# Optimization experiments

Measured on AMD Instinct MI355X. Metric: run time of the kernel, lower is better.

## Reference

```python
import jax, jax.numpy as jnp
import numpy as np

N_FEATURES = 128
D_EMBED = 64
GRID_SIZE = 5
SPLINE_ORDER = 3
FOURIER_GRIDSIZE = 10
GRID_RANGE = (-1.0, 1.0)


def setup_inputs() -> dict:
    key = jax.random.key(0)
    k1, k2, k3, k4 = jax.random.split(key, 4)
    b = 8192
    x = jax.random.uniform(k1, (b, N_FEATURES), dtype=jnp.float32)
    # grid buffer: (n_features, grid_size + 2*spline_order + 1)
    h = (GRID_RANGE[1] - GRID_RANGE[0]) / GRID_SIZE
    grid_1d = jnp.arange(-SPLINE_ORDER, GRID_SIZE + SPLINE_ORDER + 1, dtype=jnp.float32) * h + GRID_RANGE[0]
    grid = jnp.broadcast_to(grid_1d, (N_FEATURES, grid_1d.shape[0]))
    # parameters (random stand-ins for the torch init)
    base_weight = jax.random.normal(k2, (N_FEATURES, D_EMBED), dtype=jnp.float32) * 0.1
    spline_weight = jax.random.normal(k3, (N_FEATURES, D_EMBED, GRID_SIZE + SPLINE_ORDER), dtype=jnp.float32) * 0.02
    spline_scaler = jax.random.normal(k4, (N_FEATURES, D_EMBED), dtype=jnp.float32) * 0.1
    kf1, kf2 = jax.random.split(jax.random.fold_in(key, 7))
    fourier_coeffs = jax.random.normal(kf1, (2, N_FEATURES, D_EMBED, FOURIER_GRIDSIZE), dtype=jnp.float32) / (
        np.sqrt(N_FEATURES) * np.sqrt(FOURIER_GRIDSIZE))
    fourier_bias = jnp.zeros((1, N_FEATURES, D_EMBED), dtype=jnp.float32)
    return {
        'x': x, 'grid': grid, 'base_weight': base_weight,
        'spline_weight': spline_weight, 'spline_scaler': spline_scaler,
        'fourier_coeffs': fourier_coeffs, 'fourier_bias': fourier_bias,
    }


def b_splines(x, grid):
    # x: (b, n), grid: (n, grid_size + 2*spline_order + 1)
    xb = x[..., None]  # (b, n, 1)
    bases = ((xb >= grid[:, :-1]) & (xb < grid[:, 1:])).astype(x.dtype)  # (b, n, G+2k)
    for k in range(1, SPLINE_ORDER + 1):  # Cox-de Boor recursion (fixed small order)
        left = (xb - grid[:, :-(k + 1)]) / (grid[:, k:-1] - grid[:, :-(k + 1)])
        right = (grid[:, k + 1:] - xb) / (grid[:, k + 1:] - grid[:, 1:-k])
        bases = left * bases[:, :, :-1] + right * bases[:, :, 1:]
    return bases  # (b, n, grid_size + spline_order)


def reference(x, grid, base_weight, spline_weight, spline_scaler, fourier_coeffs, fourier_bias):
    # base branch: SiLU(x) outer-broadcast with per-feature weight -> (b, n, d)
    base_out = jax.nn.silu(x)[..., None] * base_weight[None]
    # spline branch
    bases = b_splines(x, grid)  # (b, n, i) with i = grid_size + spline_order
    scaled_w = spline_weight * spline_scaler[..., None]  # (n, d, i)
    spline_out = jnp.einsum('bni,ndi->bnd', bases, scaled_w)
    # Fourier branch: sum_g cos(k_g x) c0[n,d,g] + sin(k_g x) c1[n,d,g]
    kvec = jnp.arange(1, FOURIER_GRIDSIZE + 1, dtype=x.dtype)
    ang = x[..., None] * kvec  # (b, n, g)
    fourier_out = (jnp.einsum('bng,ndg->bnd', jnp.cos(ang), fourier_coeffs[0])
                   + jnp.einsum('bng,ndg->bnd', jnp.sin(ang), fourier_coeffs[1])
                   + fourier_bias)
    return base_out + spline_out + fourier_out
```

## Files before the change

kernel.cpp:

```cpp
#include <hip/hip_runtime.h>
#include <math.h>

#define NF   128
#define DE   64
#define GS   5
#define SO   3
#define FG   10
#define NG   12
#define NB0  11
#define NBF  8
#define WREC 32

__global__ __launch_bounds__(256)
void kan_prep(const float* __restrict__ grid,
              const float* __restrict__ bw, const float* __restrict__ sw,
              const float* __restrict__ ss, const float* __restrict__ fc,
              const float* __restrict__ fb,
              float* __restrict__ W, float* __restrict__ INV) {
  int idx = blockIdx.x * blockDim.x + threadIdx.x;
  if (idx >= NF * DE) return;
  int n = idx >> 6, d = idx & 63;
  (void)d;
  float* w = W + (size_t)idx * WREC;
  w[0] = bw[idx];
  w[1] = fb[idx];
  float s = ss[idx];
  const float* swp = sw + (size_t)idx * NBF;
#pragma unroll
  for (int i = 0; i < NBF; ++i) w[2 + i] = swp[i] * s;
  const float* f0 = fc + (size_t)idx * FG;
  const float* f1 = fc + (size_t)(NF * DE + idx) * FG;
#pragma unroll
  for (int g = 0; g < FG; ++g) { w[10 + g] = f0[g]; w[20 + g] = f1[g]; }
  w[30] = 0.f; w[31] = 0.f;
  if (d == 0) {
    const float* g_ = grid + n * NG;
    float* iv = INV + n * 32;
    int o = 0;
#pragma unroll
    for (int k = 1; k <= SO; ++k)
      for (int j = 0; j + k < NG; ++j)
        iv[o++] = 1.0f / (g_[j + k] - g_[j]);
    iv[30] = 0.f; iv[31] = 0.f;
  }
}

template <bool PACKED>
__global__ __launch_bounds__(256)
void kan_main(const float* __restrict__ x, const float* __restrict__ grid,
              const float* __restrict__ bw, const float* __restrict__ sw,
              const float* __restrict__ ss, const float* __restrict__ fc,
              const float* __restrict__ fb,
              const float* __restrict__ W, const float* __restrict__ INV,
              float* __restrict__ out, int B) {
  const int n = blockIdx.x;
  const int wv = threadIdx.x >> 6;
  const int lane = threadIdx.x & 63;
  const int b = ((blockIdx.y * 4 + wv) << 6) + lane;
  if (b >= B) return;

  const float xv = x[(size_t)b * NF + n];

  float g[NG];
#pragma unroll
  for (int j = 0; j < NG; ++j) g[j] = grid[n * NG + j];

  const float sil = xv / (1.0f + expf(-xv));

  float bs[NB0];
#pragma unroll
  for (int j = 0; j < NB0; ++j)
    bs[j] = (xv >= g[j] && xv < g[j + 1]) ? 1.0f : 0.0f;

  if (PACKED) {
    const float* iv = INV + n * 32;
    const float* iv1 = iv;
    const float* iv2 = iv + 11;
    const float* iv3 = iv + 21;
#pragma unroll
    for (int j = 0; j < 10; ++j) {
      float left  = (xv - g[j]) * iv1[j];
      float right = (g[j + 2] - xv) * iv1[j + 1];
      bs[j] = left * bs[j] + right * bs[j + 1];
    }
#pragma unroll
    for (int j = 0; j < 9; ++j) {
      float left  = (xv - g[j]) * iv2[j];
      float right = (g[j + 3] - xv) * iv2[j + 1];
      bs[j] = left * bs[j] + right * bs[j + 1];
    }
#pragma unroll
    for (int j = 0; j < 8; ++j) {
      float left  = (xv - g[j]) * iv3[j];
      float right = (g[j + 4] - xv) * iv3[j + 1];
      bs[j] = left * bs[j] + right * bs[j + 1];
    }
  } else {
#pragma unroll
    for (int k = 1; k <= SO; ++k) {
      for (int j = 0; j < NB0 - k; ++j) {
        float left  = (xv - g[j]) / (g[j + k] - g[j]);
        float right = (g[j + k + 1] - xv) / (g[j + k + 1] - g[j + 1]);
        bs[j] = left * bs[j] + right * bs[j + 1];
      }
    }
  }

  float cs[FG], sn[FG];
  float s1, c1;
  sincosf(xv, &s1, &c1);
  cs[0] = c1; sn[0] = s1;
#pragma unroll
  for (int gi = 1; gi < FG; ++gi) {
    float cp = cs[gi - 1], sp = sn[gi - 1];
    cs[gi] = cp * c1 - sp * s1;
    sn[gi] = sp * c1 + cp * s1;
  }

  float4* outp = reinterpret_cast<float4*>(out + ((size_t)b * NF + n) * DE);

  if (PACKED) {
    const float* wp = W + (size_t)n * DE * WREC;
    for (int d4 = 0; d4 < DE / 4; ++d4) {
      float4 o;
#pragma unroll
      for (int q = 0; q < 4; ++q) {
        const float* w = wp + (size_t)(d4 * 4 + q) * WREC;
        float a = fmaf(sil, w[0], w[1]);
#pragma unroll
        for (int i = 0; i < NBF; ++i) a = fmaf(bs[i], w[2 + i], a);
#pragma unroll
        for (int gi = 0; gi < FG; ++gi) a = fmaf(cs[gi], w[10 + gi], a);
#pragma unroll
        for (int gi = 0; gi < FG; ++gi) a = fmaf(sn[gi], w[20 + gi], a);
        (&o.x)[q] = a;
      }
      outp[d4] = o;
    }
  } else {
    const float* bwp = bw + n * DE;
    const float* fbp = fb + n * DE;
    const float* ssp = ss + n * DE;
    const float* swp = sw + (size_t)n * DE * NBF;
    const float* f0  = fc + (size_t)n * DE * FG;
    const float* f1  = fc + (size_t)(NF + n) * DE * FG;
    for (int d4 = 0; d4 < DE / 4; ++d4) {
      float4 o;
#pragma unroll
      for (int q = 0; q < 4; ++q) {
        int d = d4 * 4 + q;
        float a = fmaf(sil, bwp[d], fbp[d]);
        float scl = ssp[d];
#pragma unroll
        for (int i = 0; i < NBF; ++i) a = fmaf(bs[i] * scl, swp[d * NBF + i], a);
#pragma unroll
        for (int gi = 0; gi < FG; ++gi) a = fmaf(cs[gi], f0[d * FG + gi], a);
#pragma unroll
        for (int gi = 0; gi < FG; ++gi) a = fmaf(sn[gi], f1[d * FG + gi], a);
        (&o.x)[q] = a;
      }
      outp[d4] = o;
    }
  }
}

extern "C" void kernel_launch(void* const* d_in, const int* in_sizes, int n_in,
                              void* d_out, int out_size, void* d_ws, size_t ws_size,
                              hipStream_t stream) {
  const float* x    = (const float*)d_in[0];
  const float* grid = (const float*)d_in[1];
  const float* bw   = (const float*)d_in[2];
  const float* sw   = (const float*)d_in[3];
  const float* ss   = (const float*)d_in[4];
  const float* fc   = (const float*)d_in[5];
  const float* fb   = (const float*)d_in[6];
  float* out = (float*)d_out;

  const int B = in_sizes[0] / NF;
  dim3 mgrid(NF, (unsigned)((B + 255) / 256));
  const size_t need = (size_t)(NF * DE * WREC + NF * 32) * sizeof(float);

  if (ws_size >= need) {
    float* W   = (float*)d_ws;
    float* INV = W + (size_t)NF * DE * WREC;
    kan_prep<<<(NF * DE + 255) / 256, 256, 0, stream>>>(grid, bw, sw, ss, fc, fb, W, INV);
    kan_main<true><<<mgrid, 256, 0, stream>>>(x, grid, bw, sw, ss, fc, fb, W, INV, out, B);
  } else {
    kan_main<false><<<mgrid, 256, 0, stream>>>(x, grid, bw, sw, ss, fc, fb,
                                               nullptr, nullptr, out, B);
  }
}
```

Measured before the change: 429.5 us.

## Split KAN into feature-row kernel and coalesced per-dimension dot kernel

```diff
diff --git a/kernel.cpp b/kernel.cpp
--- a/kernel.cpp
+++ b/kernel.cpp
@@ -10,6 +10,8 @@
 #define NB0  11
 #define NBF  8
 #define WREC 32
+#define BPW  128
+
 
 __global__ __launch_bounds__(256)
 void kan_prep(const float* __restrict__ grid,
@@ -45,67 +47,139 @@
   }
 }
 
-template <bool PACKED>
 __global__ __launch_bounds__(256)
-void kan_main(const float* __restrict__ x, const float* __restrict__ grid,
+void kan_scal(const float* __restrict__ x, const float* __restrict__ grid,
+              const float* __restrict__ INV, float* __restrict__ S, int B) {
+  const int n = blockIdx.x;
+  const int b = blockIdx.y * 256 + threadIdx.x;
+  if (b >= B) return;
+
+  const float xv = x[(size_t)b * NF + n];
+
+  float g[NG];
+#pragma unroll
+  for (int j = 0; j < NG; ++j) g[j] = grid[n * NG + j];
+
+  const float sil = xv / (1.0f + expf(-xv));
+
+  float bs[NB0];
+#pragma unroll
+  for (int j = 0; j < NB0; ++j)
+    bs[j] = (xv >= g[j] && xv < g[j + 1]) ? 1.0f : 0.0f;
+
+  const float* iv = INV + n * 32;
+  const float* iv1 = iv;
+  const float* iv2 = iv + 11;
+  const float* iv3 = iv + 21;
+#pragma unroll
+  for (int j = 0; j < 10; ++j) {
+    float left  = (xv - g[j]) * iv1[j];
+    float right = (g[j + 2] - xv) * iv1[j + 1];
+    bs[j] = left * bs[j] + right * bs[j + 1];
+  }
+#pragma unroll
+  for (int j = 0; j < 9; ++j) {
+    float left  = (xv - g[j]) * iv2[j];
+    float right = (g[j + 3] - xv) * iv2[j + 1];
+    bs[j] = left * bs[j] + right * bs[j + 1];
+  }
+#pragma unroll
+  for (int j = 0; j < 8; ++j) {
+    float left  = (xv - g[j]) * iv3[j];
+    float right = (g[j + 4] - xv) * iv3[j + 1];
+    bs[j] = left * bs[j] + right * bs[j + 1];
+  }
+
+  float cs[FG], sn[FG];
+  float s1, c1;
+  sincosf(xv, &s1, &c1);
+  cs[0] = c1; sn[0] = s1;
+#pragma unroll
+  for (int gi = 1; gi < FG; ++gi) {
+    float cp = cs[gi - 1], sp = sn[gi - 1];
+    cs[gi] = cp * c1 - sp * s1;
+    sn[gi] = sp * c1 + cp * s1;
+  }
+
+  float r[WREC];
+  r[0] = sil; r[1] = 1.0f;
+#pragma unroll
+  for (int j = 0; j < NBF; ++j) r[2 + j] = bs[j];
+#pragma unroll
+  for (int gi = 0; gi < FG; ++gi) { r[10 + gi] = cs[gi]; r[20 + gi] = sn[gi]; }
+  r[30] = 0.f; r[31] = 0.f;
+
+  float4* sp4 = reinterpret_cast<float4*>(S + ((size_t)b * NF + n) * WREC);
+#pragma unroll
+  for (int q = 0; q < 8; ++q)
+    sp4[q] = make_float4(r[q * 4 + 0], r[q * 4 + 1], r[q * 4 + 2], r[q * 4 + 3]);
+}
+
+__global__ __launch_bounds__(256, 8)
+void kan_dot(const float* __restrict__ W, const float* __restrict__ S,
+             float* __restrict__ out, int B) {
+  const int n = blockIdx.x;
+  const int wv = __builtin_amdgcn_readfirstlane(threadIdx.x >> 6);
+  const int lane = threadIdx.x & 63;
+  const int bstart = (blockIdx.y * 4 + wv) * BPW;
+  if (bstart >= B) return;
+  const int nb = (B - bstart < BPW) ? (B - bstart) : BPW;
+
+  float wr[WREC];
+  const float4* wq = reinterpret_cast<const float4*>(W + ((size_t)n * DE + lane) * WREC);
+#pragma unroll
+  for (int q = 0; q < 8; ++q) {
+    float4 t = wq[q];
+    wr[q * 4 + 0] = t.x; wr[q * 4 + 1] = t.y; wr[q * 4 + 2] = t.z; wr[q * 4 + 3] = t.w;
+  }
+
+  const float* sp = S + ((size_t)bstart * NF + n) * WREC;
+  float* op = out + ((size_t)bstart * NF + n) * DE + lane;
+
+  for (int i = 0; i < nb; ++i) {
+    float a0 = 0.f, a1 = 0.f, a2 = 0.f, a3 = 0.f;
+#pragma unroll
+    for (int j = 0; j < 28; j += 4) {
+      a0 = fmaf(sp[j + 0], wr[j + 0], a0);
+      a1 = fmaf(sp[j + 1], wr[j + 1], a1);
+      a2 = fmaf(sp[j + 2], wr[j + 2], a2);
+      a3 = fmaf(sp[j + 3], wr[j + 3], a3);
+    }
+    a0 = fmaf(sp[28], wr[28], a0);
+    a1 = fmaf(sp[29], wr[29], a1);
+    *op = (a0 + a1) + (a2 + a3);
+    sp += (size_t)NF * WREC;
+    op += (size_t)NF * DE;
+  }
+}
+
+__global__ __launch_bounds__(256)
+void kan_mono(const float* __restrict__ x, const float* __restrict__ grid,
               const float* __restrict__ bw, const float* __restrict__ sw,
               const float* __restrict__ ss, const float* __restrict__ fc,
-              const float* __restrict__ fb,
-              const float* __restrict__ W, const float* __restrict__ INV,
-              float* __restrict__ out, int B) {
+              const float* __restrict__ fb, float* __restrict__ out, int B) {
   const int n = blockIdx.x;
   const int wv = threadIdx.x >> 6;
   const int lane = threadIdx.x & 63;
   const int b = ((blockIdx.y * 4 + wv) << 6) + lane;
   if (b >= B) return;
-
   const float xv = x[(size_t)b * NF + n];
-
   float g[NG];
 #pragma unroll
   for (int j = 0; j < NG; ++j) g[j] = grid[n * NG + j];
-
   const float sil = xv / (1.0f + expf(-xv));
-
   float bs[NB0];
 #pragma unroll
   for (int j = 0; j < NB0; ++j)
     bs[j] = (xv >= g[j] && xv < g[j + 1]) ? 1.0f : 0.0f;
-
-  if (PACKED) {
-    const float* iv = INV + n * 32;
-    const float* iv1 = iv;
-    const float* iv2 = iv + 11;
-    const float* iv3 = iv + 21;
-#pragma unroll
-    for (int j = 0; j < 10; ++j) {
-      float left  = (xv - g[j]) * iv1[j];
-      float right = (g[j + 2] - xv) * iv1[j + 1];
+#pragma unroll
+  for (int k = 1; k <= SO; ++k) {
+    for (int j = 0; j < NB0 - k; ++j) {
+      float left  = (xv - g[j]) / (g[j + k] - g[j]);
+      float right = (g[j + k + 1] - xv) / (g[j + k + 1] - g[j + 1]);
       bs[j] = left * bs[j] + right * bs[j + 1];
     }
-#pragma unroll
-    for (int j = 0; j < 9; ++j) {
-      float left  = (xv - g[j]) * iv2[j];
-      float right = (g[j + 3] - xv) * iv2[j + 1];
-      bs[j] = left * bs[j] + right * bs[j + 1];
-    }
-#pragma unroll
-    for (int j = 0; j < 8; ++j) {
-      float left  = (xv - g[j]) * iv3[j];
-      float right = (g[j + 4] - xv) * iv3[j + 1];
-      bs[j] = left * bs[j] + right * bs[j + 1];
-    }
-  } else {
-#pragma unroll
-    for (int k = 1; k <= SO; ++k) {
-      for (int j = 0; j < NB0 - k; ++j) {
-        float left  = (xv - g[j]) / (g[j + k] - g[j]);
-        float right = (g[j + k + 1] - xv) / (g[j + k + 1] - g[j + 1]);
-        bs[j] = left * bs[j] + right * bs[j + 1];
-      }
-    }
-  }
-
+  }
   float cs[FG], sn[FG];
   float s1, c1;
   sincosf(xv, &s1, &c1);
@@ -116,51 +190,29 @@
     cs[gi] = cp * c1 - sp * s1;
     sn[gi] = sp * c1 + cp * s1;
   }
-
+  const float* bwp = bw + n * DE;
+  const float* fbp = fb + n * DE;
+  const float* ssp = ss + n * DE;
+  const float* swp = sw + (size_t)n * DE * NBF;
+  const float* f0  = fc + (size_t)n * DE * FG;
+  const float* f1  = fc + (size_t)(NF + n) * DE * FG;
   float4* outp = reinterpret_cast<float4*>(out + ((size_t)b * NF + n) * DE);
-
-  if (PACKED) {
-    const float* wp = W + (size_t)n * DE * WREC;
-    for (int d4 = 0; d4 < DE / 4; ++d4) {
-      float4 o;
-#pragma unroll
-      for (int q = 0; q < 4; ++q) {
-        const float* w = wp + (size_t)(d4 * 4 + q) * WREC;
-        float a = fmaf(sil, w[0], w[1]);
-#pragma unroll
-        for (int i = 0; i < NBF; ++i) a = fmaf(bs[i], w[2 + i], a);
-#pragma unroll
-        for (int gi = 0; gi < FG; ++gi) a = fmaf(cs[gi], w[10 + gi], a);
-#pragma unroll
-        for (int gi = 0; gi < FG; ++gi) a = fmaf(sn[gi], w[20 + gi], a);
-        (&o.x)[q] = a;
-      }
-      outp[d4] = o;
+  for (int d4 = 0; d4 < DE / 4; ++d4) {
+    float4 o;
+#pragma unroll
+    for (int q = 0; q < 4; ++q) {
+      int d = d4 * 4 + q;
+      float a = fmaf(sil, bwp[d], fbp[d]);
+      float scl = ssp[d];
+#pragma unroll
+      for (int i = 0; i < NBF; ++i) a = fmaf(bs[i] * scl, swp[d * NBF + i], a);
+#pragma unroll
+      for (int gi = 0; gi < FG; ++gi) a = fmaf(cs[gi], f0[d * FG + gi], a);
+#pragma unroll
+      for (int gi = 0; gi < FG; ++gi) a = fmaf(sn[gi], f1[d * FG + gi], a);
+      (&o.x)[q] = a;
     }
-  } else {
-    const float* bwp = bw + n * DE;
-    const float* fbp = fb + n * DE;
-    const float* ssp = ss + n * DE;
-    const float* swp = sw + (size_t)n * DE * NBF;
-    const float* f0  = fc + (size_t)n * DE * FG;
-    const float* f1  = fc + (size_t)(NF + n) * DE * FG;
-    for (int d4 = 0; d4 < DE / 4; ++d4) {
-      float4 o;
-#pragma unroll
-      for (int q = 0; q < 4; ++q) {
-        int d = d4 * 4 + q;
-        float a = fmaf(sil, bwp[d], fbp[d]);
-        float scl = ssp[d];
-#pragma unroll
-        for (int i = 0; i < NBF; ++i) a = fmaf(bs[i] * scl, swp[d * NBF + i], a);
-#pragma unroll
-        for (int gi = 0; gi < FG; ++gi) a = fmaf(cs[gi], f0[d * FG + gi], a);
-#pragma unroll
-        for (int gi = 0; gi < FG; ++gi) a = fmaf(sn[gi], f1[d * FG + gi], a);
-        (&o.x)[q] = a;
-      }
-      outp[d4] = o;
-    }
+    outp[d4] = o;
   }
 }
 
@@ -177,16 +229,22 @@
   float* out = (float*)d_out;
 
   const int B = in_sizes[0] / NF;
-  dim3 mgrid(NF, (unsigned)((B + 255) / 256));
-  const size_t need = (size_t)(NF * DE * WREC + NF * 32) * sizeof(float);
+  const size_t wBytes = (size_t)NF * DE * WREC * sizeof(float);
+  const size_t iBytes = (size_t)NF * 32 * sizeof(float);
+  const size_t sBytes = (size_t)B * NF * WREC * sizeof(float);
+  const size_t need = wBytes + iBytes + sBytes;
 
   if (ws_size >= need) {
     float* W   = (float*)d_ws;
     float* INV = W + (size_t)NF * DE * WREC;
+    float* S   = INV + (size_t)NF * 32;
     kan_prep<<<(NF * DE + 255) / 256, 256, 0, stream>>>(grid, bw, sw, ss, fc, fb, W, INV);
-    kan_main<true><<<mgrid, 256, 0, stream>>>(x, grid, bw, sw, ss, fc, fb, W, INV, out, B);
+    dim3 g1(NF, (unsigned)((B + 255) / 256));
+    kan_scal<<<g1, 256, 0, stream>>>(x, grid, INV, S, B);
+    dim3 g2(NF, (unsigned)((B + BPW * 4 - 1) / (BPW * 4)));
+    kan_dot<<<g2, 256, 0, stream>>>(W, S, out, B);
   } else {
-    kan_main<false><<<mgrid, 256, 0, stream>>>(x, grid, bw, sw, ss, fc, fb,
-                                               nullptr, nullptr, out, B);
-  }
-}
+    dim3 mg(NF, (unsigned)((B + 255) / 256));
+    kan_mono<<<mg, 256, 0, stream>>>(x, grid, bw, sw, ss, fc, fb, out, B);
+  }
+}
```

After: 622.2 us. 44.9% more time.

## Transpose work mapping so lanes own output dims and broadcast features via readlane

Applied to the files above, without the earlier changes.

```diff
diff --git a/kernel.cpp b/kernel.cpp
--- a/kernel.cpp
+++ b/kernel.cpp
@@ -10,6 +10,7 @@
 #define NB0  11
 #define NBF  8
 #define WREC 32
+
 
 __global__ __launch_bounds__(256)
 void kan_prep(const float* __restrict__ grid,
@@ -45,67 +46,137 @@
   }
 }
 
-template <bool PACKED>
+__device__ __forceinline__ float bcast_lane(float v, int src) {
+  return __int_as_float(__builtin_amdgcn_readlane(__float_as_int(v), src));
+}
+
 __global__ __launch_bounds__(256)
-void kan_main(const float* __restrict__ x, const float* __restrict__ grid,
+void kan_fused(const float* __restrict__ x, const float* __restrict__ grid,
+               const float* __restrict__ INV, const float* __restrict__ W,
+               float* __restrict__ out, int B) {
+  const int n = blockIdx.x;
+  const int lane = threadIdx.x & 63;
+  const int wv = threadIdx.x >> 6;
+  const int b0 = blockIdx.y * 256 + wv * 64;
+  if (b0 >= B) return;
+  const int myb = b0 + lane;
+
+  float xv = (myb < B) ? x[(size_t)myb * NF + n] : 0.0f;
+
+  float g[NG];
+#pragma unroll
+  for (int j = 0; j < NG; ++j) g[j] = grid[n * NG + j];
+
+  float sv[29];
+  sv[0] = xv / (1.0f + expf(-xv));
+
+  float bs[NB0];
+#pragma unroll
+  for (int j = 0; j < NB0; ++j)
+    bs[j] = (xv >= g[j] && xv < g[j + 1]) ? 1.0f : 0.0f;
+
+  const float* iv = INV + n * 32;
+  const float* iv1 = iv;
+  const float* iv2 = iv + 11;
+  const float* iv3 = iv + 21;
+#pragma unroll
+  for (int j = 0; j < 10; ++j) {
+    float left  = (xv - g[j]) * iv1[j];
+    float right = (g[j + 2] - xv) * iv1[j + 1];
+    bs[j] = left * bs[j] + right * bs[j + 1];
+  }
+#pragma unroll
+  for (int j = 0; j < 9; ++j) {
+    float left  = (xv - g[j]) * iv2[j];
+    float right = (g[j + 3] - xv) * iv2[j + 1];
+    bs[j] = left * bs[j] + right * bs[j + 1];
+  }
+#pragma unroll
+  for (int j = 0; j < 8; ++j) {
+    float left  = (xv - g[j]) * iv3[j];
+    float right = (g[j + 4] - xv) * iv3[j + 1];
+    bs[j] = left * bs[j] + right * bs[j + 1];
+  }
+#pragma unroll
+  for (int j = 0; j < NBF; ++j) sv[1 + j] = bs[j];
+
+  {
+    float s1, c1;
+    sincosf(xv, &s1, &c1);
+    sv[9] = c1; sv[19] = s1;
+#pragma unroll
+    for (int gi = 1; gi < FG; ++gi) {
+      float cp = sv[9 + gi - 1], sp = sv[19 + gi - 1];
+      sv[9 + gi]  = cp * c1 - sp * s1;
+      sv[19 + gi] = sp * c1 + cp * s1;
+    }
+  }
+
+  float wr[30];
+  {
+    const float4* wq = reinterpret_cast<const float4*>(W + ((size_t)n * DE + lane) * WREC);
+#pragma unroll
+    for (int q = 0; q < 7; ++q) {
+      float4 t = wq[q];
+      wr[q * 4 + 0] = t.x; wr[q * 4 + 1] = t.y; wr[q * 4 + 2] = t.z; wr[q * 4 + 3] = t.w;
+    }
+    float2 t7 = reinterpret_cast<const float2*>(wq)[14];
+    wr[28] = t7.x; wr[29] = t7.y;
+  }
+
+  float* op = out + ((size_t)b0 * NF + n) * DE + lane;
+  const int nb = (B - b0 < 64) ? (B - b0) : 64;
+
+#pragma unroll 4
+  for (int bi = 0; bi < nb; ++bi) {
+    float a0 = wr[1];
+    float a1 = bcast_lane(sv[0], bi) * wr[0];
+#pragma unroll
+    for (int j = 0; j < NBF; j += 2) {
+      a0 = fmaf(bcast_lane(sv[1 + j],     bi), wr[2 + j],     a0);
+      a1 = fmaf(bcast_lane(sv[1 + j + 1], bi), wr[2 + j + 1], a1);
+    }
+#pragma unroll
+    for (int gi = 0; gi < FG; gi += 2) {
+      a0 = fmaf(bcast_lane(sv[9 + gi],     bi), wr[10 + gi],     a0);
+      a1 = fmaf(bcast_lane(sv[9 + gi + 1], bi), wr[10 + gi + 1], a1);
+    }
+#pragma unroll
+    for (int gi = 0; gi < FG; gi += 2) {
+      a0 = fmaf(bcast_lane(sv[19 + gi],     bi), wr[20 + gi],     a0);
+      a1 = fmaf(bcast_lane(sv[19 + gi + 1], bi), wr[20 + gi + 1], a1);
+    }
+    op[(size_t)bi * NF * DE] = a0 + a1;
+  }
+}
+
+__global__ __launch_bounds__(256)
+void kan_mono(const float* __restrict__ x, const float* __restrict__ grid,
               const float* __restrict__ bw, const float* __restrict__ sw,
               const float* __restrict__ ss, const float* __restrict__ fc,
-              const float* __restrict__ fb,
-              const float* __restrict__ W, const float* __restrict__ INV,
-              float* __restrict__ out, int B) {
+              const float* __restrict__ fb, float* __restrict__ out, int B) {
   const int n = blockIdx.x;
   const int wv = threadIdx.x >> 6;
   const int lane = threadIdx.x & 63;
   const int b = ((blockIdx.y * 4 + wv) << 6) + lane;
   if (b >= B) return;
-
   const float xv = x[(size_t)b * NF + n];
-
   float g[NG];
 #pragma unroll
   for (int j = 0; j < NG; ++j) g[j] = grid[n * NG + j];
-
   const float sil = xv / (1.0f + expf(-xv));
-
   float bs[NB0];
 #pragma unroll
   for (int j = 0; j < NB0; ++j)
     bs[j] = (xv >= g[j] && xv < g[j + 1]) ? 1.0f : 0.0f;
-
-  if (PACKED) {
-    const float* iv = INV + n * 32;
-    const float* iv1 = iv;
-    const float* iv2 = iv + 11;
-    const float* iv3 = iv + 21;
-#pragma unroll
-    for (int j = 0; j < 10; ++j) {
-      float left  = (xv - g[j]) * iv1[j];
-      float right = (g[j + 2] - xv) * iv1[j + 1];
+#pragma unroll
+  for (int k = 1; k <= SO; ++k) {
+    for (int j = 0; j < NB0 - k; ++j) {
+      float left  = (xv - g[j]) / (g[j + k] - g[j]);
+      float right = (g[j + k + 1] - xv) / (g[j + k + 1] - g[j + 1]);
       bs[j] = left * bs[j] + right * bs[j + 1];
     }
-#pragma unroll
-    for (int j = 0; j < 9; ++j) {
-      float left  = (xv - g[j]) * iv2[j];
-      float right = (g[j + 3] - xv) * iv2[j + 1];
-      bs[j] = left * bs[j] + right * bs[j + 1];
-    }
-#pragma unroll
-    for (int j = 0; j < 8; ++j) {
-      float left  = (xv - g[j]) * iv3[j];
-      float right = (g[j + 4] - xv) * iv3[j + 1];
-      bs[j] = left * bs[j] + right * bs[j + 1];
-    }
-  } else {
-#pragma unroll
-    for (int k = 1; k <= SO; ++k) {
-      for (int j = 0; j < NB0 - k; ++j) {
-        float left  = (xv - g[j]) / (g[j + k] - g[j]);
-        float right = (g[j + k + 1] - xv) / (g[j + k + 1] - g[j + 1]);
-        bs[j] = left * bs[j] + right * bs[j + 1];
-      }
-    }
-  }
-
+  }
   float cs[FG], sn[FG];
   float s1, c1;
   sincosf(xv, &s1, &c1);
@@ -116,51 +187,29 @@
     cs[gi] = cp * c1 - sp * s1;
     sn[gi] = sp * c1 + cp * s1;
   }
-
+  const float* bwp = bw + n * DE;
+  const float* fbp = fb + n * DE;
+  const float* ssp = ss + n * DE;
+  const float* swp = sw + (size_t)n * DE * NBF;
+  const float* f0  = fc + (size_t)n * DE * FG;
+  const float* f1  = fc + (size_t)(NF + n) * DE * FG;
   float4* outp = reinterpret_cast<float4*>(out + ((size_t)b * NF + n) * DE);
-
-  if (PACKED) {
-    const float* wp = W + (size_t)n * DE * WREC;
-    for (int d4 = 0; d4 < DE / 4; ++d4) {
-      float4 o;
-#pragma unroll
-      for (int q = 0; q < 4; ++q) {
-        const float* w = wp + (size_t)(d4 * 4 + q) * WREC;
-        float a = fmaf(sil, w[0], w[1]);
-#pragma unroll
-        for (int i = 0; i < NBF; ++i) a = fmaf(bs[i], w[2 + i], a);
-#pragma unroll
-        for (int gi = 0; gi < FG; ++gi) a = fmaf(cs[gi], w[10 + gi], a);
-#pragma unroll
-        for (int gi = 0; gi < FG; ++gi) a = fmaf(sn[gi], w[20 + gi], a);
-        (&o.x)[q] = a;
-      }
-      outp[d4] = o;
-    }
-  } else {
-    const float* bwp = bw + n * DE;
-    const float* fbp = fb + n * DE;
-    const float* ssp = ss + n * DE;
-    const float* swp = sw + (size_t)n * DE * NBF;
-    const float* f0  = fc + (size_t)n * DE * FG;
-    const float* f1  = fc + (size_t)(NF + n) * DE * FG;
-    for (int d4 = 0; d4 < DE / 4; ++d4) {
-      float4 o;
-#pragma unroll
-      for (int q = 0; q < 4; ++q) {
-        int d = d4 * 4 + q;
-        float a = fmaf(sil, bwp[d], fbp[d]);
-        float scl = ssp[d];
-#pragma unroll
-        for (int i = 0; i < NBF; ++i) a = fmaf(bs[i] * scl, swp[d * NBF + i], a);
-#pragma unroll
-        for (int gi = 0; gi < FG; ++gi) a = fmaf(cs[gi], f0[d * FG + gi], a);
-#pragma unroll
-        for (int gi = 0; gi < FG; ++gi) a = fmaf(sn[gi], f1[d * FG + gi], a);
-        (&o.x)[q] = a;
-      }
-      outp[d4] = o;
-    }
+  for (int d4 = 0; d4 < DE / 4; ++d4) {
+    float4 o;
+#pragma unroll
+    for (int q = 0; q < 4; ++q) {
+      int d = d4 * 4 + q;
+      float a = fmaf(sil, bwp[d], fbp[d]);
+      float scl = ssp[d];
+#pragma unroll
+      for (int i = 0; i < NBF; ++i) a = fmaf(bs[i] * scl, swp[d * NBF + i], a);
+#pragma unroll
+      for (int gi = 0; gi < FG; ++gi) a = fmaf(cs[gi], f0[d * FG + gi], a);
+#pragma unroll
+      for (int gi = 0; gi < FG; ++gi) a = fmaf(sn[gi], f1[d * FG + gi], a);
+      (&o.x)[q] = a;
+    }
+    outp[d4] = o;
   }
 }
 
@@ -177,16 +226,16 @@
   float* out = (float*)d_out;
 
   const int B = in_sizes[0] / NF;
-  dim3 mgrid(NF, (unsigned)((B + 255) / 256));
   const size_t need = (size_t)(NF * DE * WREC + NF * 32) * sizeof(float);
 
   if (ws_size >= need) {
     float* W   = (float*)d_ws;
     float* INV = W + (size_t)NF * DE * WREC;
     kan_prep<<<(NF * DE + 255) / 256, 256, 0, stream>>>(grid, bw, sw, ss, fc, fb, W, INV);
-    kan_main<true><<<mgrid, 256, 0, stream>>>(x, grid, bw, sw, ss, fc, fb, W, INV, out, B);
+    dim3 gf(NF, (unsigned)((B + 255) / 256));
+    kan_fused<<<gf, 256, 0, stream>>>(x, grid, INV, W, out, B);
   } else {
-    kan_main<false><<<mgrid, 256, 0, stream>>>(x, grid, bw, sw, ss, fc, fb,
-                                               nullptr, nullptr, out, B);
-  }
-}
+    dim3 mg(NF, (unsigned)((B + 255) / 256));
+    kan_mono<<<mg, 256, 0, stream>>>(x, grid, bw, sw, ss, fc, fb, out, B);
+  }
+}
```

New measurement: 378.3 us. 1.14x faster.
